# Kernel optimization log

Measured on AMD Instinct MI355X. Metric: run time of the kernel, lower is better.

## Reference

```python
import jax, jax.numpy as jnp
import numpy as np

N = 100000   # nodes (in_ch)
D = 128      # emb_ch
E = 1600000  # nonzeros in A_hat
RATE = 0.1   # dropout rate


def setup_inputs() -> dict:
    key = jax.random.key(0)
    k1, k2, k3, k4, k5, k6 = jax.random.split(key, 6)
    x = jnp.arange(N, dtype=jnp.int64) if jax.config.jax_enable_x64 else jnp.arange(N, dtype=jnp.int32)
    rows = jax.random.randint(k1, (E,), 0, N)
    cols = jax.random.randint(k2, (E,), 0, N)
    A_vals = jax.random.uniform(k3, (E,), dtype=jnp.float32)
    # xavier_uniform for [N, D]: bound = sqrt(6/(N+D))
    bound = float(np.sqrt(6.0 / (N + D)))
    emb_weight = jax.random.uniform(k4, (N, D), jnp.float32, -bound, bound)
    u1 = jax.random.uniform(k5, (N, D), dtype=jnp.float32)
    u2 = jax.random.uniform(k6, (N, D), dtype=jnp.float32)
    return {"x": x, "rows": rows, "cols": cols, "A_vals": A_vals,
            "emb_weight": emb_weight, "u1": u1, "u2": u2}


def _dropout(h, u):
    keep = (u >= RATE).astype(h.dtype)
    return h * keep / (1.0 - RATE)


def _spmm(rows, cols, vals, h):
    # out[i] = sum_{e: rows[e]==i} vals[e] * h[cols[e]]  -- COO SpMM
    msgs = vals[:, None] * h[cols]  # [E, D]
    return jax.ops.segment_sum(msgs, rows, num_segments=N)


def reference(x, rows, cols, A_vals, emb_weight, u1, u2):
    h0 = emb_weight[x]                       # embedding lookup [N, D]
    h1 = _spmm(rows, cols, A_vals, _dropout(h0, u1))
    h2 = _spmm(rows, cols, A_vals, _dropout(h1, u2))
    return (h0 + h1 + h2) / 3.0
```

## Files before the change

### kernel.cpp

```cpp
#include <hip/hip_runtime.h>
#include <hip/hip_fp16.h>

#define DD 128
#define SCAN_CHUNK 1024

typedef float          f32x4 __attribute__((ext_vector_type(4)));
typedef unsigned int   u32x4 __attribute__((ext_vector_type(4)));
typedef unsigned int   u32x2 __attribute__((ext_vector_type(2)));
typedef unsigned short u16x8 __attribute__((ext_vector_type(8)));

struct __align__(8) Edge { int c; float v; };

__device__ __forceinline__ unsigned short f2h(float f) {
    return __half_as_ushort(__float2half(f));
}
__device__ __forceinline__ float2 up2(unsigned int u) {
    __half2 h = *reinterpret_cast<const __half2*>(&u);
    return __half22float2(h);
}

template <typename T>
__device__ __forceinline__ T ldnt(const T* p) { return __builtin_nontemporal_load(p); }
template <typename T>
__device__ __forceinline__ void stnt(T* p, T v) { __builtin_nontemporal_store(v, p); }


__global__ __launch_bounds__(256) void k_zero(int* __restrict__ p, int n) {
    int i = blockIdx.x * 256 + threadIdx.x;
    if (i < n) p[i] = 0;
}

__global__ __launch_bounds__(256) void k_hist(const int* __restrict__ rows,
                                              int* __restrict__ cnt,
                                              int* __restrict__ rank, int E) {
    int e = blockIdx.x * 256 + threadIdx.x;
    if (e < E) {
        int r = ldnt(rows + e);
        int old = atomicAdd(&cnt[r], 1);
        stnt(rank + e, old);
    }
}

__global__ __launch_bounds__(256) void k_scan1(int* __restrict__ data,
                                               int* __restrict__ bsum, int n) {
    __shared__ int s[256];
    int tid = threadIdx.x;
    int base = blockIdx.x * SCAN_CHUNK + tid * 4;
    int v0 = 0, v1 = 0, v2 = 0, v3 = 0;
    if (base + 0 < n) v0 = data[base + 0];
    if (base + 1 < n) v1 = data[base + 1];
    if (base + 2 < n) v2 = data[base + 2];
    if (base + 3 < n) v3 = data[base + 3];
    int tsum = v0 + v1 + v2 + v3;
    s[tid] = tsum;
    __syncthreads();
    for (int off = 1; off < 256; off <<= 1) {
        int t = (tid >= off) ? s[tid - off] : 0;
        __syncthreads();
        s[tid] += t;
        __syncthreads();
    }
    int excl = s[tid] - tsum;
    if (tid == 255) bsum[blockIdx.x] = s[255];
    if (base + 0 < n) data[base + 0] = excl;
    if (base + 1 < n) data[base + 1] = excl + v0;
    if (base + 2 < n) data[base + 2] = excl + v0 + v1;
    if (base + 3 < n) data[base + 3] = excl + v0 + v1 + v2;
}

__global__ __launch_bounds__(256) void k_scan23(int* __restrict__ data,
                                                const int* __restrict__ bsum,
                                                int nb, int n) {
    __shared__ int s[1024];
    int tid = threadIdx.x;
    for (int i = tid; i < nb; i += 256) s[i] = bsum[i];
    __syncthreads();
    if (tid == 0) {
        int run = 0;
        for (int i = 0; i < nb; ++i) { int t = s[i]; s[i] = run; run += t; }
    }
    __syncthreads();
    int i = blockIdx.x * 256 + tid;
    if (i < n) data[i] += s[i >> 10];
}

__global__ __launch_bounds__(256) void k_scatter(const int* __restrict__ rows,
                                                 const int* __restrict__ cols,
                                                 const float* __restrict__ vals,
                                                 const int* __restrict__ rowstart,
                                                 const int* __restrict__ rank,
                                                 Edge* __restrict__ ev, int E) {
    int e = blockIdx.x * 256 + threadIdx.x;
    if (e >= E) return;
    int r = ldnt(rows + e);
    Edge ed;
    ed.c = ldnt(cols + e);
    ed.v = ldnt(vals + e);
    ev[rowstart[r] + rank[e]] = ed;
}


__global__ __launch_bounds__(256) void k_drop_h(const float* __restrict__ src,
                                                const float* __restrict__ u,
                                                ushort* __restrict__ g, int total8) {
    int i = blockIdx.x * 256 + threadIdx.x;
    if (i >= total8) return;
    const f32x4* s4 = (const f32x4*)src;
    const f32x4* u4 = (const f32x4*)u;
    f32x4 hA = ldnt(s4 + 2 * (size_t)i);
    f32x4 hB = ldnt(s4 + 2 * (size_t)i + 1);
    f32x4 uA = ldnt(u4 + 2 * (size_t)i);
    f32x4 uB = ldnt(u4 + 2 * (size_t)i + 1);
    const float s = 1.0f / 0.9f;
    u16x8 o;
    o[0] = f2h((uA.x >= 0.1f) ? hA.x * s : 0.0f);
    o[1] = f2h((uA.y >= 0.1f) ? hA.y * s : 0.0f);
    o[2] = f2h((uA.z >= 0.1f) ? hA.z * s : 0.0f);
    o[3] = f2h((uA.w >= 0.1f) ? hA.w * s : 0.0f);
    o[4] = f2h((uB.x >= 0.1f) ? hB.x * s : 0.0f);
    o[5] = f2h((uB.y >= 0.1f) ? hB.y * s : 0.0f);
    o[6] = f2h((uB.z >= 0.1f) ? hB.z * s : 0.0f);
    o[7] = f2h((uB.w >= 0.1f) ? hB.w * s : 0.0f);
    ((u16x8*)g)[i] = o;
}

template <int MODE>
__global__ __launch_bounds__(256) void k_gather(const int* __restrict__ rowstart,
                                                const Edge* __restrict__ ev,
                                                const ushort* __restrict__ srch,
                                                const float* __restrict__ u2,
                                                const float* __restrict__ emb,
                                                const ushort* __restrict__ p16in,
                                                ushort* __restrict__ p16out,
                                                ushort* __restrict__ g2,
                                                float* __restrict__ out,
                                                int N, int E) {
    int t = blockIdx.x * 256 + threadIdx.x;
    int row = t >> 4;
    int lane = t & 15;
    if (row >= N) return;
    int start = rowstart[row];
    int end = (row == N - 1) ? E : rowstart[row + 1];
    const u32x4* __restrict__ s4 = (const u32x4*)srch;
    float a0 = 0.f, a1 = 0.f, a2 = 0.f, a3 = 0.f;
    float a4 = 0.f, a5 = 0.f, a6 = 0.f, a7 = 0.f;

#define LDE(i) Edge E##i; { u32x2 q_ = ldnt((const u32x2*)(ev + e + i)); \
                            E##i.c = (int)q_.x; E##i.v = __uint_as_float(q_.y); }
#define GQ(i)  u32x4 q##i = s4[((size_t)E##i.c << 4) + lane];
#define ACC(i) { float vv = E##i.v; \
        float2 w0 = up2(q##i.x), w1 = up2(q##i.y), w2 = up2(q##i.z), w3 = up2(q##i.w); \
        a0 = fmaf(vv, w0.x, a0); a1 = fmaf(vv, w0.y, a1); \
        a2 = fmaf(vv, w1.x, a2); a3 = fmaf(vv, w1.y, a3); \
        a4 = fmaf(vv, w2.x, a4); a5 = fmaf(vv, w2.y, a5); \
        a6 = fmaf(vv, w3.x, a6); a7 = fmaf(vv, w3.y, a7); }

    int e = start;
    for (; e + 8 <= end; e += 8) {
        LDE(0) LDE(1) LDE(2) LDE(3) LDE(4) LDE(5) LDE(6) LDE(7)
        GQ(0) GQ(1) GQ(2) GQ(3) GQ(4) GQ(5) GQ(6) GQ(7)
        ACC(0) ACC(1) ACC(2) ACC(3) ACC(4) ACC(5) ACC(6) ACC(7)
    }
    if (e + 4 <= end) {
        LDE(0) LDE(1) LDE(2) LDE(3)
        GQ(0) GQ(1) GQ(2) GQ(3)
        ACC(0) ACC(1) ACC(2) ACC(3)
        e += 4;
    }
    for (; e < end; ++e) {
        LDE(0) GQ(0) ACC(0)
    }
#undef LDE
#undef GQ
#undef ACC

    size_t o = ((size_t)row << 7) + (size_t)lane * 8;
    if (MODE == 1) {
        const f32x4* u4 = (const f32x4*)(u2 + o);
        f32x4 uA = ldnt(u4);
        f32x4 uB = ldnt(u4 + 1);
        const float s = 1.0f / 0.9f;
        u16x8 gg;
        gg[0] = f2h((uA.x >= 0.1f) ? a0 * s : 0.0f);
        gg[1] = f2h((uA.y >= 0.1f) ? a1 * s : 0.0f);
        gg[2] = f2h((uA.z >= 0.1f) ? a2 * s : 0.0f);
        gg[3] = f2h((uA.w >= 0.1f) ? a3 * s : 0.0f);
        gg[4] = f2h((uB.x >= 0.1f) ? a4 * s : 0.0f);
        gg[5] = f2h((uB.y >= 0.1f) ? a5 * s : 0.0f);
        gg[6] = f2h((uB.z >= 0.1f) ? a6 * s : 0.0f);
        gg[7] = f2h((uB.w >= 0.1f) ? a7 * s : 0.0f);
        stnt((u16x8*)(g2 + o), gg);
        u16x8 pp;
        pp[0] = f2h(a0); pp[1] = f2h(a1); pp[2] = f2h(a2); pp[3] = f2h(a3);
        pp[4] = f2h(a4); pp[5] = f2h(a5); pp[6] = f2h(a6); pp[7] = f2h(a7);
        stnt((u16x8*)(p16out + o), pp);
    } else {
        f32x4 eA = ldnt((const f32x4*)(emb + o));
        f32x4 eB = ldnt((const f32x4*)(emb + o) + 1);
        u32x4 pq = ldnt((const u32x4*)(p16in + o));
        float2 p0 = up2(pq.x), p1 = up2(pq.y), p2 = up2(pq.z), p3 = up2(pq.w);
        const float t3 = 1.0f / 3.0f;
        f32x4 rA, rB;
        rA.x = (eA.x + p0.x + a0) * t3;
        rA.y = (eA.y + p0.y + a1) * t3;
        rA.z = (eA.z + p1.x + a2) * t3;
        rA.w = (eA.w + p1.y + a3) * t3;
        rB.x = (eB.x + p2.x + a4) * t3;
        rB.y = (eB.y + p2.y + a5) * t3;
        rB.z = (eB.z + p3.x + a6) * t3;
        rB.w = (eB.w + p3.y + a7) * t3;
        stnt((f32x4*)(out + o), rA);
        stnt((f32x4*)(out + o) + 1, rB);
    }
}


extern "C" void kernel_launch(void* const* d_in, const int* in_sizes, int n_in,
                              void* d_out, int out_size, void* d_ws, size_t ws_size,
                              hipStream_t stream) {
    const int* rows = (const int*)d_in[1];
    const int* cols = (const int*)d_in[2];
    const float* vals = (const float*)d_in[3];
    const float* emb = (const float*)d_in[4];
    const float* u1 = (const float*)d_in[5];
    const float* u2 = (const float*)d_in[6];
    float* out = (float*)d_out;

    const int N = in_sizes[0];
    const int E = in_sizes[1];
    const size_t ND = (size_t)N * DD;

    char* ws = (char*)d_ws;
    ushort* g1  = (ushort*)ws; ws += ND * sizeof(ushort);
    ushort* g2  = (ushort*)ws; ws += ND * sizeof(ushort);
    ushort* p16 = (ushort*)ws; ws += ND * sizeof(ushort);
    int* cnt    = (int*)ws;    ws += (size_t)N * sizeof(int);
    int* rank   = (int*)ws;    ws += (size_t)E * sizeof(int);
    Edge* ev    = (Edge*)ws;   ws += (size_t)E * sizeof(Edge);
    int* bsum   = (int*)ws;

    const int total8 = (int)(ND / 8);
    const int gridDrop = (total8 + 255) / 256;
    const int gridE = (E + 255) / 256;
    const int gridN = (N + 255) / 256;
    const int nScanBlocks = (N + SCAN_CHUNK - 1) / SCAN_CHUNK;
    const int gridRow = (int)(((size_t)N * 16 + 255) / 256);

    k_zero<<<gridN, 256, 0, stream>>>(cnt, N);
    k_hist<<<gridE, 256, 0, stream>>>(rows, cnt, rank, E);
    k_scan1<<<nScanBlocks, 256, 0, stream>>>(cnt, bsum, N);
    k_scan23<<<gridN, 256, 0, stream>>>(cnt, bsum, nScanBlocks, N);
    k_scatter<<<gridE, 256, 0, stream>>>(rows, cols, vals, cnt, rank, ev, E);

    k_drop_h<<<gridDrop, 256, 0, stream>>>(emb, u1, g1, total8);
    k_gather<1><<<gridRow, 256, 0, stream>>>(cnt, ev, g1, u2, nullptr, nullptr,
                                             p16, g2, nullptr, N, E);
    k_gather<2><<<gridRow, 256, 0, stream>>>(cnt, ev, g2, nullptr, emb, p16,
                                             nullptr, nullptr, out, N, E);
}
```

Before: 439.4 us.

## Fuse prep with histogram, pack dropout mask, stage edges in LDS, fp16 embedding

Merges the dropout and fp16 conversion of the embedding with the row histogram into one launch. It also precomputes a bitmask for the second dropout and an fp16 copy of the embedding, so the gather kernels read less data. The scatter now takes slots through an atomic cursor instead of a stored rank array, and the gather stages each block's edge list in shared memory. The costs are nondeterministic edge order within a row, reduced precision on the embedding term of the output, and an extra sync per block.

After: 455.7 us. +3.7%, slower.

```diff
diff --git a/kernel.cpp b/kernel.cpp
--- a/kernel.cpp
+++ b/kernel.cpp
@@ -3,6 +3,8 @@
 
 #define DD 128
 #define SCAN_CHUNK 1024
+#define ROWS_PER_BLK 16
+#define MAX_STAGE 512
 
 typedef float          f32x4 __attribute__((ext_vector_type(4)));
 typedef unsigned int   u32x4 __attribute__((ext_vector_type(4)));
@@ -30,14 +32,54 @@
     if (i < n) p[i] = 0;
 }
 
-__global__ __launch_bounds__(256) void k_hist(const int* __restrict__ rows,
-                                              int* __restrict__ cnt,
-                                              int* __restrict__ rank, int E) {
-    int e = blockIdx.x * 256 + threadIdx.x;
-    if (e < E) {
-        int r = ldnt(rows + e);
-        int old = atomicAdd(&cnt[r], 1);
-        stnt(rank + e, old);
+__global__ __launch_bounds__(256) void k_prep(const float* __restrict__ emb,
+                                              const float* __restrict__ u1,
+                                              const float* __restrict__ u2,
+                                              ushort* __restrict__ g1,
+                                              ushort* __restrict__ emb16,
+                                              unsigned char* __restrict__ mask2,
+                                              int total8, int prepBlocks,
+                                              const int* __restrict__ rows,
+                                              int* __restrict__ cnt, int E) {
+    if ((int)blockIdx.x < prepBlocks) {
+        int i = blockIdx.x * 256 + threadIdx.x;
+        if (i >= total8) return;
+        const f32x4* e4 = (const f32x4*)emb;
+        const f32x4* a4 = (const f32x4*)u1;
+        const f32x4* b4 = (const f32x4*)u2;
+        f32x4 hA = ldnt(e4 + 2 * (size_t)i);
+        f32x4 hB = ldnt(e4 + 2 * (size_t)i + 1);
+        f32x4 uA = ldnt(a4 + 2 * (size_t)i);
+        f32x4 uB = ldnt(a4 + 2 * (size_t)i + 1);
+        f32x4 vA = ldnt(b4 + 2 * (size_t)i);
+        f32x4 vB = ldnt(b4 + 2 * (size_t)i + 1);
+        const float s = 1.0f / 0.9f;
+        u16x8 g;
+        g[0] = f2h((uA.x >= 0.1f) ? hA.x * s : 0.0f);
+        g[1] = f2h((uA.y >= 0.1f) ? hA.y * s : 0.0f);
+        g[2] = f2h((uA.z >= 0.1f) ? hA.z * s : 0.0f);
+        g[3] = f2h((uA.w >= 0.1f) ? hA.w * s : 0.0f);
+        g[4] = f2h((uB.x >= 0.1f) ? hB.x * s : 0.0f);
+        g[5] = f2h((uB.y >= 0.1f) ? hB.y * s : 0.0f);
+        g[6] = f2h((uB.z >= 0.1f) ? hB.z * s : 0.0f);
+        g[7] = f2h((uB.w >= 0.1f) ? hB.w * s : 0.0f);
+        ((u16x8*)g1)[i] = g;
+        u16x8 e16;
+        e16[0] = f2h(hA.x); e16[1] = f2h(hA.y); e16[2] = f2h(hA.z); e16[3] = f2h(hA.w);
+        e16[4] = f2h(hB.x); e16[5] = f2h(hB.y); e16[6] = f2h(hB.z); e16[7] = f2h(hB.w);
+        stnt((u16x8*)emb16 + i, e16);
+        unsigned char m =
+            (unsigned char)((vA.x >= 0.1f ? 1u : 0u)  | (vA.y >= 0.1f ? 2u : 0u)  |
+                            (vA.z >= 0.1f ? 4u : 0u)  | (vA.w >= 0.1f ? 8u : 0u)  |
+                            (vB.x >= 0.1f ? 16u : 0u) | (vB.y >= 0.1f ? 32u : 0u) |
+                            (vB.z >= 0.1f ? 64u : 0u) | (vB.w >= 0.1f ? 128u : 0u));
+        stnt(mask2 + i, m);
+    } else {
+        int e = ((int)blockIdx.x - prepBlocks) * 256 + threadIdx.x;
+        if (e < E) {
+            int r = ldnt(rows + e);
+            atomicAdd(&cnt[r], 1);
+        }
     }
 }
 
@@ -70,6 +112,7 @@
 
 __global__ __launch_bounds__(256) void k_scan23(int* __restrict__ data,
                                                 const int* __restrict__ bsum,
+                                                int* __restrict__ cursor,
                                                 int nb, int n) {
     __shared__ int s[1024];
     int tid = threadIdx.x;
@@ -81,72 +124,75 @@
     }
     __syncthreads();
     int i = blockIdx.x * 256 + tid;
-    if (i < n) data[i] += s[i >> 10];
+    if (i < n) {
+        int v = data[i] + s[i >> 10];
+        data[i] = v;
+        cursor[i] = v;
+    }
 }
 
 __global__ __launch_bounds__(256) void k_scatter(const int* __restrict__ rows,
                                                  const int* __restrict__ cols,
                                                  const float* __restrict__ vals,
-                                                 const int* __restrict__ rowstart,
-                                                 const int* __restrict__ rank,
+                                                 int* __restrict__ cursor,
                                                  Edge* __restrict__ ev, int E) {
     int e = blockIdx.x * 256 + threadIdx.x;
     if (e >= E) return;
     int r = ldnt(rows + e);
-    Edge ed;
-    ed.c = ldnt(cols + e);
-    ed.v = ldnt(vals + e);
-    ev[rowstart[r] + rank[e]] = ed;
-}
-
-
-__global__ __launch_bounds__(256) void k_drop_h(const float* __restrict__ src,
-                                                const float* __restrict__ u,
-                                                ushort* __restrict__ g, int total8) {
-    int i = blockIdx.x * 256 + threadIdx.x;
-    if (i >= total8) return;
-    const f32x4* s4 = (const f32x4*)src;
-    const f32x4* u4 = (const f32x4*)u;
-    f32x4 hA = ldnt(s4 + 2 * (size_t)i);
-    f32x4 hB = ldnt(s4 + 2 * (size_t)i + 1);
-    f32x4 uA = ldnt(u4 + 2 * (size_t)i);
-    f32x4 uB = ldnt(u4 + 2 * (size_t)i + 1);
-    const float s = 1.0f / 0.9f;
-    u16x8 o;
-    o[0] = f2h((uA.x >= 0.1f) ? hA.x * s : 0.0f);
-    o[1] = f2h((uA.y >= 0.1f) ? hA.y * s : 0.0f);
-    o[2] = f2h((uA.z >= 0.1f) ? hA.z * s : 0.0f);
-    o[3] = f2h((uA.w >= 0.1f) ? hA.w * s : 0.0f);
-    o[4] = f2h((uB.x >= 0.1f) ? hB.x * s : 0.0f);
-    o[5] = f2h((uB.y >= 0.1f) ? hB.y * s : 0.0f);
-    o[6] = f2h((uB.z >= 0.1f) ? hB.z * s : 0.0f);
-    o[7] = f2h((uB.w >= 0.1f) ? hB.w * s : 0.0f);
-    ((u16x8*)g)[i] = o;
+    int c = ldnt(cols + e);
+    float v = ldnt(vals + e);
+    int pos = atomicAdd(&cursor[r], 1);
+    u32x2 q;
+    q.x = (unsigned int)c;
+    q.y = __float_as_uint(v);
+    ((u32x2*)ev)[pos] = q;
 }
 
 template <int MODE>
 __global__ __launch_bounds__(256) void k_gather(const int* __restrict__ rowstart,
                                                 const Edge* __restrict__ ev,
                                                 const ushort* __restrict__ srch,
-                                                const float* __restrict__ u2,
-                                                const float* __restrict__ emb,
+                                                const unsigned char* __restrict__ mask2,
+                                                const ushort* __restrict__ emb16,
                                                 const ushort* __restrict__ p16in,
                                                 ushort* __restrict__ p16out,
                                                 ushort* __restrict__ g2,
                                                 float* __restrict__ out,
                                                 int N, int E) {
-    int t = blockIdx.x * 256 + threadIdx.x;
-    int row = t >> 4;
-    int lane = t & 15;
+    __shared__ int s_rs[ROWS_PER_BLK + 1];
+    __shared__ Edge s_ev[MAX_STAGE];
+
+    int tid = threadIdx.x;
+    int r0 = blockIdx.x * ROWS_PER_BLK;
+    if (tid <= ROWS_PER_BLK) {
+        int r = r0 + tid;
+        s_rs[tid] = (r < N) ? rowstart[r] : E;
+    }
+    __syncthreads();
+    int base = s_rs[0];
+    int nblk = s_rs[ROWS_PER_BLK] - base;
+    int nstage = nblk < MAX_STAGE ? nblk : MAX_STAGE;
+    for (int i = tid; i < nstage; i += 256) {
+        u32x2 q = ldnt((const u32x2*)(ev + base + i));
+        Edge ed; ed.c = (int)q.x; ed.v = __uint_as_float(q.y);
+        s_ev[i] = ed;
+    }
+    __syncthreads();
+
+    int grp = tid >> 4;
+    int lane = tid & 15;
+    int row = r0 + grp;
     if (row >= N) return;
-    int start = rowstart[row];
-    int end = (row == N - 1) ? E : rowstart[row + 1];
+    int start = s_rs[grp] - base;
+    int end = s_rs[grp + 1] - base;
+    int eL = end < nstage ? end : nstage;
+
     const u32x4* __restrict__ s4 = (const u32x4*)srch;
+    const Edge* __restrict__ evg = ev + base;
     float a0 = 0.f, a1 = 0.f, a2 = 0.f, a3 = 0.f;
     float a4 = 0.f, a5 = 0.f, a6 = 0.f, a7 = 0.f;
 
-#define LDE(i) Edge E##i; { u32x2 q_ = ldnt((const u32x2*)(ev + e + i)); \
-                            E##i.c = (int)q_.x; E##i.v = __uint_as_float(q_.y); }
+#define LDE(i) Edge E##i = s_ev[e + i];
 #define GQ(i)  u32x4 q##i = s4[((size_t)E##i.c << 4) + lane];
 #define ACC(i) { float vv = E##i.v; \
         float2 w0 = up2(q##i.x), w1 = up2(q##i.y), w2 = up2(q##i.z), w3 = up2(q##i.w); \
@@ -156,19 +202,24 @@
         a6 = fmaf(vv, w3.x, a6); a7 = fmaf(vv, w3.y, a7); }
 
     int e = start;
-    for (; e + 8 <= end; e += 8) {
+    for (; e + 8 <= eL; e += 8) {
         LDE(0) LDE(1) LDE(2) LDE(3) LDE(4) LDE(5) LDE(6) LDE(7)
         GQ(0) GQ(1) GQ(2) GQ(3) GQ(4) GQ(5) GQ(6) GQ(7)
         ACC(0) ACC(1) ACC(2) ACC(3) ACC(4) ACC(5) ACC(6) ACC(7)
     }
-    if (e + 4 <= end) {
+    if (e + 4 <= eL) {
         LDE(0) LDE(1) LDE(2) LDE(3)
         GQ(0) GQ(1) GQ(2) GQ(3)
         ACC(0) ACC(1) ACC(2) ACC(3)
         e += 4;
     }
+    for (; e < eL; ++e) {
+        LDE(0) GQ(0) ACC(0)
+    }
     for (; e < end; ++e) {
-        LDE(0) GQ(0) ACC(0)
+        Edge E0; { u32x2 q_ = ldnt((const u32x2*)(evg + e));
+                   E0.c = (int)q_.x; E0.v = __uint_as_float(q_.y); }
+        GQ(0) ACC(0)
     }
 #undef LDE
 #undef GQ
@@ -176,39 +227,37 @@
 
     size_t o = ((size_t)row << 7) + (size_t)lane * 8;
     if (MODE == 1) {
-        const f32x4* u4 = (const f32x4*)(u2 + o);
-        f32x4 uA = ldnt(u4);
-        f32x4 uB = ldnt(u4 + 1);
+        unsigned int m = ldnt(mask2 + (size_t)row * 16 + lane);
         const float s = 1.0f / 0.9f;
         u16x8 gg;
-        gg[0] = f2h((uA.x >= 0.1f) ? a0 * s : 0.0f);
-        gg[1] = f2h((uA.y >= 0.1f) ? a1 * s : 0.0f);
-        gg[2] = f2h((uA.z >= 0.1f) ? a2 * s : 0.0f);
-        gg[3] = f2h((uA.w >= 0.1f) ? a3 * s : 0.0f);
-        gg[4] = f2h((uB.x >= 0.1f) ? a4 * s : 0.0f);
-        gg[5] = f2h((uB.y >= 0.1f) ? a5 * s : 0.0f);
-        gg[6] = f2h((uB.z >= 0.1f) ? a6 * s : 0.0f);
-        gg[7] = f2h((uB.w >= 0.1f) ? a7 * s : 0.0f);
+        gg[0] = (m & 1u)   ? f2h(a0 * s) : (ushort)0;
+        gg[1] = (m & 2u)   ? f2h(a1 * s) : (ushort)0;
+        gg[2] = (m & 4u)   ? f2h(a2 * s) : (ushort)0;
+        gg[3] = (m & 8u)   ? f2h(a3 * s) : (ushort)0;
+        gg[4] = (m & 16u)  ? f2h(a4 * s) : (ushort)0;
+        gg[5] = (m & 32u)  ? f2h(a5 * s) : (ushort)0;
+        gg[6] = (m & 64u)  ? f2h(a6 * s) : (ushort)0;
+        gg[7] = (m & 128u) ? f2h(a7 * s) : (ushort)0;
         stnt((u16x8*)(g2 + o), gg);
         u16x8 pp;
         pp[0] = f2h(a0); pp[1] = f2h(a1); pp[2] = f2h(a2); pp[3] = f2h(a3);
         pp[4] = f2h(a4); pp[5] = f2h(a5); pp[6] = f2h(a6); pp[7] = f2h(a7);
         stnt((u16x8*)(p16out + o), pp);
     } else {
-        f32x4 eA = ldnt((const f32x4*)(emb + o));
-        f32x4 eB = ldnt((const f32x4*)(emb + o) + 1);
+        u32x4 eq = ldnt((const u32x4*)(emb16 + o));
         u32x4 pq = ldnt((const u32x4*)(p16in + o));
+        float2 e0 = up2(eq.x), e1 = up2(eq.y), e2 = up2(eq.z), e3 = up2(eq.w);
         float2 p0 = up2(pq.x), p1 = up2(pq.y), p2 = up2(pq.z), p3 = up2(pq.w);
         const float t3 = 1.0f / 3.0f;
         f32x4 rA, rB;
-        rA.x = (eA.x + p0.x + a0) * t3;
-        rA.y = (eA.y + p0.y + a1) * t3;
-        rA.z = (eA.z + p1.x + a2) * t3;
-        rA.w = (eA.w + p1.y + a3) * t3;
-        rB.x = (eB.x + p2.x + a4) * t3;
-        rB.y = (eB.y + p2.y + a5) * t3;
-        rB.z = (eB.z + p3.x + a6) * t3;
-        rB.w = (eB.w + p3.y + a7) * t3;
+        rA.x = (e0.x + p0.x + a0) * t3;
+        rA.y = (e0.y + p0.y + a1) * t3;
+        rA.z = (e1.x + p1.x + a2) * t3;
+        rA.w = (e1.y + p1.y + a3) * t3;
+        rB.x = (e2.x + p2.x + a4) * t3;
+        rB.y = (e2.y + p2.y + a5) * t3;
+        rB.z = (e3.x + p3.x + a6) * t3;
+        rB.w = (e3.y + p3.y + a7) * t3;
         stnt((f32x4*)(out + o), rA);
         stnt((f32x4*)(out + o) + 1, rB);
     }
@@ -231,30 +280,32 @@
     const size_t ND = (size_t)N * DD;
 
     char* ws = (char*)d_ws;
-    ushort* g1  = (ushort*)ws; ws += ND * sizeof(ushort);
-    ushort* g2  = (ushort*)ws; ws += ND * sizeof(ushort);
-    ushort* p16 = (ushort*)ws; ws += ND * sizeof(ushort);
-    int* cnt    = (int*)ws;    ws += (size_t)N * sizeof(int);
-    int* rank   = (int*)ws;    ws += (size_t)E * sizeof(int);
-    Edge* ev    = (Edge*)ws;   ws += (size_t)E * sizeof(Edge);
-    int* bsum   = (int*)ws;
+    Edge* ev     = (Edge*)ws;   ws += (size_t)E * sizeof(Edge);
+    ushort* g1   = (ushort*)ws; ws += ND * sizeof(ushort);
+    ushort* g2   = (ushort*)ws; ws += ND * sizeof(ushort);
+    ushort* p16  = (ushort*)ws; ws += ND * sizeof(ushort);
+    ushort* emb16= (ushort*)ws; ws += ND * sizeof(ushort);
+    int* cnt     = (int*)ws;    ws += (size_t)N * sizeof(int);
+    int* cursor  = (int*)ws;    ws += (size_t)N * sizeof(int);
+    int* bsum    = (int*)ws;    ws += 4096;
+    unsigned char* mask2 = (unsigned char*)ws;
 
     const int total8 = (int)(ND / 8);
-    const int gridDrop = (total8 + 255) / 256;
+    const int prepBlocks = (total8 + 255) / 256;
     const int gridE = (E + 255) / 256;
     const int gridN = (N + 255) / 256;
     const int nScanBlocks = (N + SCAN_CHUNK - 1) / SCAN_CHUNK;
-    const int gridRow = (int)(((size_t)N * 16 + 255) / 256);
+    const int gridRow = (N + ROWS_PER_BLK - 1) / ROWS_PER_BLK;
 
     k_zero<<<gridN, 256, 0, stream>>>(cnt, N);
-    k_hist<<<gridE, 256, 0, stream>>>(rows, cnt, rank, E);
+    k_prep<<<prepBlocks + gridE, 256, 0, stream>>>(emb, u1, u2, g1, emb16, mask2,
+                                                   total8, prepBlocks, rows, cnt, E);
     k_scan1<<<nScanBlocks, 256, 0, stream>>>(cnt, bsum, N);
-    k_scan23<<<gridN, 256, 0, stream>>>(cnt, bsum, nScanBlocks, N);
-    k_scatter<<<gridE, 256, 0, stream>>>(rows, cols, vals, cnt, rank, ev, E);
-
-    k_drop_h<<<gridDrop, 256, 0, stream>>>(emb, u1, g1, total8);
-    k_gather<1><<<gridRow, 256, 0, stream>>>(cnt, ev, g1, u2, nullptr, nullptr,
+    k_scan23<<<gridN, 256, 0, stream>>>(cnt, bsum, cursor, nScanBlocks, N);
+    k_scatter<<<gridE, 256, 0, stream>>>(rows, cols, vals, cursor, ev, E);
+
+    k_gather<1><<<gridRow, 256, 0, stream>>>(cnt, ev, g1, mask2, nullptr, nullptr,
                                              p16, g2, nullptr, N, E);
-    k_gather<2><<<gridRow, 256, 0, stream>>>(cnt, ev, g2, nullptr, emb, p16,
+    k_gather<2><<<gridRow, 256, 0, stream>>>(cnt, ev, g2, nullptr, emb16, p16,
                                              nullptr, nullptr, out, N, E);
 }
```
